# Kernel optimization log

Hardware: AMD Instinct MI355X
Metric: run time of the kernel (lower is better)

The kernel has to match this reference:

```python
import jax, jax.numpy as jnp
import numpy as np
from jax import lax

EPS = 1e-4  # BatchNorm2d eps
K, STRIDE, PAD = 3, 1, 1


def _conv_nchw(x, w, stride, pad):
    return lax.conv_general_dilated(
        x, w, window_strides=(stride, stride), padding=[(pad, pad), (pad, pad)],
        dimension_numbers=("NCHW", "OIHW", "NCHW"))


def setup_inputs() -> dict:
    key = jax.random.key(0)
    ks = jax.random.split(key, 6)
    N, C, H, W = 16, 256, 56, 56
    Cout = 256
    return {
        "x": jax.random.normal(ks[0], (N, C, H, W), jnp.float32),
        "bn_gamma": jax.random.uniform(ks[1], (C,), jnp.float32, 0.5, 1.5),
        "bn_beta": jax.random.normal(ks[2], (C,), jnp.float32) * 0.1,
        "conv_w": jax.random.normal(ks[3], (Cout, C, K, K), jnp.float32) * (1.0 / np.sqrt(C * K * K)),
        "conv_b": jax.random.normal(ks[4], (Cout,), jnp.float32) * 0.01,
        "beta_conv_b": jax.random.normal(ks[5], (1,), jnp.float32) * 0.01,
    }


def reference(x, bn_gamma, bn_beta, conv_w, conv_b, beta_conv_b):
    # --- BatchNorm2d (training-mode batch stats, affine) ---
    mean = jnp.mean(x, axis=(0, 2, 3), keepdims=True)
    var = jnp.mean(jnp.square(x - mean), axis=(0, 2, 3), keepdims=True)  # biased
    xn = (x - mean) * lax.rsqrt(var + EPS)
    xn = xn * bn_gamma[None, :, None, None] + bn_beta[None, :, None, None]

    # --- Ternary quantize (threshold=0; le overwrites ge, so x==0 -> -1) ---
    t = jnp.where(xn >= 0.0, 1.0, 0.0)
    t = jnp.where(xn <= 0.0, -1.0, t).astype(xn.dtype)
    # scale=True, clamp=True
    xc = jnp.clip(xn, -1.0, 1.0)
    c_sum = jnp.sum(xc * t, axis=1, keepdims=True)       # [N,1,H,W]
    c_cnt = jnp.sum(jnp.abs(t), axis=1, keepdims=True)   # L1 norm over channels

    # --- Main conv on ternary activations ---
    y = _conv_nchw(t, conv_w, STRIDE, PAD) + conv_b[None, :, None, None]

    # --- beta: ones-weight box filter (+ beta_conv bias) ---
    ones_k = jnp.ones((1, 1, K, K), x.dtype)
    b_sum = _conv_nchw(c_sum, ones_k, STRIDE, PAD) + beta_conv_b[0]
    b_cnt = _conv_nchw(c_cnt, ones_k, STRIDE, PAD) + beta_conv_b[0]
    beta_map = b_sum / b_cnt                             # [N,1,Ho,Wo]
    return y * beta_map
```

## Files before the change

kernel.cpp:

```cpp
#include <hip/hip_runtime.h>
#include <hip/hip_bf16.h>

typedef __attribute__((ext_vector_type(8))) short bf16x8;
typedef __attribute__((ext_vector_type(4))) float f32x4;

#define NB 16
#define C 256
#define HH 56
#define WW 56
#define HW 3136
#define CHW 802816
#define NPIX 50176
#define PH 58
#define PW 58
#define KTOT 2304
#define PPI 3364
#define NPIXP 53824

#define GLL(g, l) __builtin_amdgcn_global_load_lds( \
    (const __attribute__((address_space(1))) void*)(g), \
    (__attribute__((address_space(3))) void*)(l), 16, 0, 0)

__global__ __launch_bounds__(1024) void stats_kernel(const float* __restrict__ x,
                             const float* __restrict__ gamma, double* __restrict__ stats) {
  int c = blockIdx.x, tid = threadIdx.x;
  double s = 0.0, s2 = 0.0;
  const float* xc = x + (size_t)c * HW;
  for (int k = tid; k < NB * (HW / 4); k += 1024) {
    int n = k / (HW / 4), i = k - n * (HW / 4);
    float4 v = *(const float4*)(xc + (size_t)n * CHW + i * 4);
    double a = v.x, b = v.y, cc = v.z, d = v.w;
    s  += (a + b) + (cc + d);
    s2 += (a * a + b * b) + (cc * cc + d * d);
  }
  __shared__ double rs[1024], rq[1024];
  rs[tid] = s; rq[tid] = s2; __syncthreads();
  for (int o = 512; o > 0; o >>= 1) {
    if (tid < o) { rs[tid] += rs[tid + o]; rq[tid] += rq[tid + o]; }
    __syncthreads();
  }
  if (tid == 0) {
    double mean = rs[0] / (double)NPIX;
    double var = rq[0] / (double)NPIX - mean * mean;
    stats[c] = mean;
    stats[C + c] = (double)gamma[c] / sqrt(var + 1e-4);
  }
}

__global__ __launch_bounds__(256) void ternarize_kernel(const float* __restrict__ x,
                                 const float* __restrict__ beta,
                                 const double* __restrict__ stats,
                                 unsigned short* __restrict__ Tp, float* __restrict__ csum) {
  int bid = blockIdx.x, tid = threadIdx.x;
  int n = bid / HH, h = bid - n * HH;
  __shared__ float xs[256][57];
  const float* xb = x + (size_t)n * CHW + h * WW;
#pragma unroll
  for (int j = 0; j < 14; ++j) {
    int idx = j * 256 + tid;
    int c = idx / 14, q = idx - c * 14;
    float4 v = *(const float4*)(xb + (size_t)c * HW + q * 4);
    float* row = &xs[c][q * 4];
    row[0] = v.x; row[1] = v.y; row[2] = v.z; row[3] = v.w;
  }
  int c8 = tid & 31;
  double mu[8], sc[8], bt[8];
#pragma unroll
  for (int e = 0; e < 8; ++e) {
    int c = c8 + 32 * e;
    mu[e] = stats[c]; sc[e] = stats[C + c]; bt[e] = (double)beta[c];
  }
  __syncthreads();
  unsigned short* tb = Tp + ((size_t)(n * PH + h + 1) * PW + 1) * C;
  float* cs = csum + (size_t)(n * PH + h + 1) * PW + 1;
#pragma unroll
  for (int p = 0; p < 7; ++p) {
    int idx = p * 256 + tid;
    int w = idx >> 5;
    unsigned bits[4];
    float msum = 0.f;
#pragma unroll
    for (int e2 = 0; e2 < 4; ++e2) {
      unsigned lo, hi;
      {
        double xn = ((double)xs[c8 + 64 * e2][w] - mu[2 * e2]) * sc[2 * e2] + bt[2 * e2];
        lo = (xn > 0.0) ? 0x3F80u : 0xBF80u;
        msum += (float)fmin(fabs(xn), 1.0);
      }
      {
        double xn = ((double)xs[c8 + 64 * e2 + 32][w] - mu[2 * e2 + 1]) * sc[2 * e2 + 1] + bt[2 * e2 + 1];
        hi = (xn > 0.0) ? 0x3F80u : 0xBF80u;
        msum += (float)fmin(fabs(xn), 1.0);
      }
      bits[e2] = lo | (hi << 16);
    }
    msum += __shfl_xor(msum, 1); msum += __shfl_xor(msum, 2);
    msum += __shfl_xor(msum, 4); msum += __shfl_xor(msum, 8);
    msum += __shfl_xor(msum, 16);
    uint4 v4; v4.x = bits[0]; v4.y = bits[1]; v4.z = bits[2]; v4.w = bits[3];
    *(uint4*)(tb + (size_t)w * C + c8 * 8) = v4;
    if (c8 == 0) cs[w] = msum;
  }
}

__global__ void prep_kernel(const float* __restrict__ cw, unsigned short* __restrict__ Wp,
                            unsigned short* __restrict__ Tp, float* __restrict__ csum) {
  int b = blockIdx.x, tid = threadIdx.x;
  if (b < 256) {
    int co = b;
    const float* src = cw + (size_t)co * KTOT;
    unsigned short* dst = Wp + (size_t)co * KTOT;
    float v[9];
#pragma unroll
    for (int t9 = 0; t9 < 9; ++t9) v[t9] = src[tid * 9 + t9];
    int p = (tid & 31) * 8 + (tid >> 5);
#pragma unroll
    for (int t9 = 0; t9 < 9; ++t9) {
      unsigned u = __builtin_bit_cast(unsigned, v[t9]);
      unsigned lsb = (u >> 16) & 1u;
      u += 0x7FFFu + lsb;
      dst[t9 * 256 + p] = (unsigned short)(u >> 16);
    }
  } else if (b < 712) {
    int g = (b - 256) * 256 + tid;
    int n = g / 7296; int r = g - n * 7296;
    int pix = r >> 5, c8 = r & 31;
    int h, w;
    if (pix < 58)      { h = 0;  w = pix; }
    else if (pix < 116){ h = 57; w = pix - 58; }
    else { int rem = pix - 116; h = 1 + (rem >> 1); w = (rem & 1) ? 57 : 0; }
    uint4 z = {0u, 0u, 0u, 0u};
    *(uint4*)(Tp + (size_t)((n * PH + h) * PW + w) * C + c8 * 8) = z;
  } else {
    int i = (b - 712) * 256 + tid;
    if (i < NPIXP) csum[i] = 0.f;
  }
}

__global__ __launch_bounds__(512, 2) void conv_kernel(const unsigned short* __restrict__ Wp,
    const unsigned short* __restrict__ Tp, const float* __restrict__ convb,
    const float* __restrict__ csum, const float* __restrict__ betab,
    float* __restrict__ out) {
  int bid = blockIdx.x;
  int ptg = bid >> 5, xcd = bid & 7, ct = (bid >> 3) & 3;
  int pt = ptg * 8 + xcd;
  if (pt >= 106) return;
  int tid = threadIdx.x;
  int co0 = ct * 64;

  __shared__ __align__(16) unsigned short As[2][18432];
  __shared__ __align__(16) unsigned short Bs[2][20480];

  int aofs[5];
#pragma unroll
  for (int r = 0; r < 5; ++r) {
    int lin = r * 512 + tid;
    int co = (lin >> 2) & 63, tap = lin >> 8, pseg = lin & 3;
    int lseg = pseg ^ ((co >> 1) & 3);
    aofs[r] = (co0 + co) * KTOT + tap * 256 + lseg * 8;
  }
  int wstart = pt * 512 - 59;
  int bofs[5];
#pragma unroll
  for (int r = 0; r < 5; ++r) {
    int lin = r * 512 + tid;
    int bpix = lin >> 2, pseg = lin & 3;
    int lseg = pseg ^ ((bpix >> 1) & 3);
    int q = wstart + bpix;
    q = q < 0 ? 0 : (q >= NPIXP ? NPIXP - 1 : q);
    bofs[r] = q * C + lseg * 8;
  }

  int lane = tid & 63, wid = tid >> 6;
  int quad = lane >> 4, row16 = lane & 15;
  int aFoff = row16 * 32 + (quad ^ ((row16 >> 1) & 3)) * 8;
  int pixb = wid * 64 + row16;

  f32x4 acc[4][4];
#pragma unroll
  for (int mi = 0; mi < 4; ++mi)
#pragma unroll
    for (int ni = 0; ni < 4; ++ni)
      acc[mi][ni] = (f32x4){0.f, 0.f, 0.f, 0.f};

#pragma unroll
  for (int r = 0; r < 4; ++r) GLL(Wp + aofs[r], &As[0][(r * 512 + tid) * 8]);
  if (tid < 256)               GLL(Wp + aofs[4], &As[0][(2048 + tid) * 8]);
#pragma unroll
  for (int r = 0; r < 5; ++r) GLL(Tp + bofs[r], &Bs[0][(r * 512 + tid) * 8]);

  for (int s = 0; s < 8; ++s) {
    int cur = s & 1;
    __syncthreads();
    if (s < 7) {
      int c0n = (s + 1) * 32;
#pragma unroll
      for (int r = 0; r < 4; ++r) GLL(Wp + aofs[r] + c0n, &As[cur ^ 1][(r * 512 + tid) * 8]);
      if (tid < 256)               GLL(Wp + aofs[4] + c0n, &As[cur ^ 1][(2048 + tid) * 8]);
#pragma unroll
      for (int r = 0; r < 5; ++r) GLL(Tp + bofs[r] + c0n, &Bs[cur ^ 1][(r * 512 + tid) * 8]);
    }
    const unsigned short* aB = &As[cur][0];
    const unsigned short* bB = &Bs[cur][0];
    __builtin_amdgcn_s_setprio(1);
#pragma unroll
    for (int kh = 0; kh < 3; ++kh) {
#pragma unroll
      for (int kw = 0; kw < 3; ++kw) {
        int tap = kh * 3 + kw;
        bf16x8 a[4], b[4];
#pragma unroll
        for (int mi = 0; mi < 4; ++mi)
          a[mi] = *(const bf16x8*)(aB + tap * 2048 + mi * 512 + aFoff);
#pragma unroll
        for (int ni = 0; ni < 4; ++ni) {
          int pix = pixb + ni * 16 + kh * 58 + kw;
          b[ni] = *(const bf16x8*)(bB + pix * 32 + ((quad ^ ((pix >> 1) & 3)) * 8));
        }
#pragma unroll
        for (int mi = 0; mi < 4; ++mi)
#pragma unroll
          for (int ni = 0; ni < 4; ++ni)
            acc[mi][ni] = __builtin_amdgcn_mfma_f32_16x16x32_bf16(a[mi], b[ni], acc[mi][ni], 0, 0, 0);
      }
    }
    __builtin_amdgcn_s_setprio(0);
  }

  float bb = betab[0];
#pragma unroll
  for (int ni = 0; ni < 4; ++ni) {
    int pp = pt * 512 + wid * 64 + ni * 16 + row16;
    if (pp >= NPIXP) continue;
    int n = pp / PPI; int r2 = pp - n * PPI;
    int ph = r2 / PW;  int pw = r2 - ph * PW;
    if (ph < 1 || ph > 56 || pw < 1 || pw > 56) continue;
    const float* cp = csum + (size_t)(n * PH + ph - 1) * PW + (pw - 1);
    float s9 = 0.f;
#pragma unroll
    for (int i = 0; i < 3; ++i)
#pragma unroll
      for (int j = 0; j < 3; ++j) s9 += cp[i * PW + j];
    int rows = 3 - (ph == 1) - (ph == 56);
    int cols = 3 - (pw == 1) - (pw == 56);
    float bm = (s9 + bb) / (256.0f * (float)(rows * cols) + bb);
    int pix = (ph - 1) * WW + (pw - 1);
    float* ob = out + (size_t)n * CHW + pix;
#pragma unroll
    for (int mi = 0; mi < 4; ++mi) {
      int co = co0 + mi * 16 + quad * 4;
#pragma unroll
      for (int rg = 0; rg < 4; ++rg) {
        ob[(size_t)(co + rg) * HW] = (acc[mi][ni][rg] + convb[co + rg]) * bm;
      }
    }
  }
}

extern "C" void kernel_launch(void* const* d_in, const int* in_sizes, int n_in,
                              void* d_out, int out_size, void* d_ws, size_t ws_size,
                              hipStream_t stream) {
  const float* x     = (const float*)d_in[0];
  const float* gamma = (const float*)d_in[1];
  const float* beta  = (const float*)d_in[2];
  const float* convw = (const float*)d_in[3];
  const float* convb = (const float*)d_in[4];
  const float* betab = (const float*)d_in[5];
  float* out = (float*)d_out;

  char* ws = (char*)d_ws;
  unsigned short* Tp   = (unsigned short*)(ws);
  unsigned short* Wp   = (unsigned short*)(ws + 27557888);
  float*          csum = (float*)(ws + 28737536);
  double*         stats= (double*)(ws + 29153536);

  prep_kernel<<<923, 256, 0, stream>>>(convw, Wp, Tp, csum);
  stats_kernel<<<256, 1024, 0, stream>>>(x, gamma, stats);
  ternarize_kernel<<<896, 256, 0, stream>>>(x, beta, stats, Tp, csum);
  conv_kernel<<<448, 512, 0, stream>>>(Wp, Tp, convb, csum, betab, out);
}
```

Before: 195.7 us.

## Shrink conv tile to 256 pixels with per-kernel-row K staging; merge prep and stats

The conv kernel moves from 512-thread blocks over 512 padded pixels to 256-thread blocks over 256 pixels. The K loop becomes 24 stages, one per kernel row and 32-channel slice, and each stage stages only the three kw taps plus a 320-pixel window. This cuts LDS use per block sharply, raising occupancy and the number of blocks, at the cost of more barriers and more re-fetching of overlapping input rows. Separately, the weight-prep and BN-stats kernels are merged into one launch to remove a kernel launch boundary.

```diff
diff --git a/kernel.cpp b/kernel.cpp
--- a/kernel.cpp
+++ b/kernel.cpp
@@ -21,108 +21,49 @@
     (const __attribute__((address_space(1))) void*)(g), \
     (__attribute__((address_space(3))) void*)(l), 16, 0, 0)
 
-__global__ __launch_bounds__(1024) void stats_kernel(const float* __restrict__ x,
-                             const float* __restrict__ gamma, double* __restrict__ stats) {
-  int c = blockIdx.x, tid = threadIdx.x;
-  double s = 0.0, s2 = 0.0;
-  const float* xc = x + (size_t)c * HW;
-  for (int k = tid; k < NB * (HW / 4); k += 1024) {
-    int n = k / (HW / 4), i = k - n * (HW / 4);
-    float4 v = *(const float4*)(xc + (size_t)n * CHW + i * 4);
-    double a = v.x, b = v.y, cc = v.z, d = v.w;
-    s  += (a + b) + (cc + d);
-    s2 += (a * a + b * b) + (cc * cc + d * d);
-  }
-  __shared__ double rs[1024], rq[1024];
-  rs[tid] = s; rq[tid] = s2; __syncthreads();
-  for (int o = 512; o > 0; o >>= 1) {
-    if (tid < o) { rs[tid] += rs[tid + o]; rq[tid] += rq[tid + o]; }
-    __syncthreads();
-  }
-  if (tid == 0) {
-    double mean = rs[0] / (double)NPIX;
-    double var = rq[0] / (double)NPIX - mean * mean;
-    stats[c] = mean;
-    stats[C + c] = (double)gamma[c] / sqrt(var + 1e-4);
-  }
-}
-
-__global__ __launch_bounds__(256) void ternarize_kernel(const float* __restrict__ x,
-                                 const float* __restrict__ beta,
-                                 const double* __restrict__ stats,
-                                 unsigned short* __restrict__ Tp, float* __restrict__ csum) {
-  int bid = blockIdx.x, tid = threadIdx.x;
-  int n = bid / HH, h = bid - n * HH;
-  __shared__ float xs[256][57];
-  const float* xb = x + (size_t)n * CHW + h * WW;
-#pragma unroll
-  for (int j = 0; j < 14; ++j) {
-    int idx = j * 256 + tid;
-    int c = idx / 14, q = idx - c * 14;
-    float4 v = *(const float4*)(xb + (size_t)c * HW + q * 4);
-    float* row = &xs[c][q * 4];
-    row[0] = v.x; row[1] = v.y; row[2] = v.z; row[3] = v.w;
-  }
-  int c8 = tid & 31;
-  double mu[8], sc[8], bt[8];
-#pragma unroll
-  for (int e = 0; e < 8; ++e) {
-    int c = c8 + 32 * e;
-    mu[e] = stats[c]; sc[e] = stats[C + c]; bt[e] = (double)beta[c];
-  }
-  __syncthreads();
-  unsigned short* tb = Tp + ((size_t)(n * PH + h + 1) * PW + 1) * C;
-  float* cs = csum + (size_t)(n * PH + h + 1) * PW + 1;
-#pragma unroll
-  for (int p = 0; p < 7; ++p) {
-    int idx = p * 256 + tid;
-    int w = idx >> 5;
-    unsigned bits[4];
-    float msum = 0.f;
-#pragma unroll
-    for (int e2 = 0; e2 < 4; ++e2) {
-      unsigned lo, hi;
-      {
-        double xn = ((double)xs[c8 + 64 * e2][w] - mu[2 * e2]) * sc[2 * e2] + bt[2 * e2];
-        lo = (xn > 0.0) ? 0x3F80u : 0xBF80u;
-        msum += (float)fmin(fabs(xn), 1.0);
-      }
-      {
-        double xn = ((double)xs[c8 + 64 * e2 + 32][w] - mu[2 * e2 + 1]) * sc[2 * e2 + 1] + bt[2 * e2 + 1];
-        hi = (xn > 0.0) ? 0x3F80u : 0xBF80u;
-        msum += (float)fmin(fabs(xn), 1.0);
-      }
-      bits[e2] = lo | (hi << 16);
-    }
-    msum += __shfl_xor(msum, 1); msum += __shfl_xor(msum, 2);
-    msum += __shfl_xor(msum, 4); msum += __shfl_xor(msum, 8);
-    msum += __shfl_xor(msum, 16);
-    uint4 v4; v4.x = bits[0]; v4.y = bits[1]; v4.z = bits[2]; v4.w = bits[3];
-    *(uint4*)(tb + (size_t)w * C + c8 * 8) = v4;
-    if (c8 == 0) cs[w] = msum;
-  }
-}
-
-__global__ void prep_kernel(const float* __restrict__ cw, unsigned short* __restrict__ Wp,
-                            unsigned short* __restrict__ Tp, float* __restrict__ csum) {
+__global__ __launch_bounds__(1024) void prep_stats_kernel(const float* __restrict__ x,
+                             const float* __restrict__ gamma, const float* __restrict__ cw,
+                             double* __restrict__ stats, unsigned short* __restrict__ Wp,
+                             unsigned short* __restrict__ Tp, float* __restrict__ csum) {
   int b = blockIdx.x, tid = threadIdx.x;
   if (b < 256) {
-    int co = b;
-    const float* src = cw + (size_t)co * KTOT;
+    int c = b;
+    double s = 0.0, s2 = 0.0;
+    const float* xc = x + (size_t)c * HW;
+    for (int k = tid; k < NB * (HW / 4); k += 1024) {
+      int n = k / (HW / 4), i = k - n * (HW / 4);
+      float4 v = *(const float4*)(xc + (size_t)n * CHW + i * 4);
+      double a = v.x, bb = v.y, cc = v.z, d = v.w;
+      s  += (a + bb) + (cc + d);
+      s2 += (a * a + bb * bb) + (cc * cc + d * d);
+    }
+    __shared__ double rs[1024], rq[1024];
+    rs[tid] = s; rq[tid] = s2; __syncthreads();
+    for (int o = 512; o > 0; o >>= 1) {
+      if (tid < o) { rs[tid] += rs[tid + o]; rq[tid] += rq[tid + o]; }
+      __syncthreads();
+    }
+    if (tid == 0) {
+      double mean = rs[0] / (double)NPIX;
+      double var = rq[0] / (double)NPIX - mean * mean;
+      stats[c] = mean;
+      stats[C + c] = (double)gamma[c] / sqrt(var + 1e-4);
+    }
+  } else if (b < 320) {
+    int co = (b - 256) * 4 + (tid >> 8);
+    int c  = tid & 255;
+    const float* src = cw + (size_t)co * KTOT + c * 9;
     unsigned short* dst = Wp + (size_t)co * KTOT;
-    float v[9];
-#pragma unroll
-    for (int t9 = 0; t9 < 9; ++t9) v[t9] = src[tid * 9 + t9];
-    int p = (tid & 31) * 8 + (tid >> 5);
+    int p = (c & 31) * 8 + (c >> 5);
 #pragma unroll
     for (int t9 = 0; t9 < 9; ++t9) {
-      unsigned u = __builtin_bit_cast(unsigned, v[t9]);
+      unsigned u = __builtin_bit_cast(unsigned, src[t9]);
       unsigned lsb = (u >> 16) & 1u;
       u += 0x7FFFu + lsb;
       dst[t9 * 256 + p] = (unsigned short)(u >> 16);
     }
-  } else if (b < 712) {
-    int g = (b - 256) * 256 + tid;
+  } else if (b < 434) {
+    int g = (b - 320) * 1024 + tid;
     int n = g / 7296; int r = g - n * 7296;
     int pix = r >> 5, c8 = r & 31;
     int h, w;
@@ -132,49 +73,101 @@
     uint4 z = {0u, 0u, 0u, 0u};
     *(uint4*)(Tp + (size_t)((n * PH + h) * PW + w) * C + c8 * 8) = z;
   } else {
-    int i = (b - 712) * 256 + tid;
+    int i = (b - 434) * 1024 + tid;
     if (i < NPIXP) csum[i] = 0.f;
   }
 }
 
-__global__ __launch_bounds__(512, 2) void conv_kernel(const unsigned short* __restrict__ Wp,
+__global__ __launch_bounds__(256) void ternarize_kernel(const float* __restrict__ x,
+                                 const float* __restrict__ beta,
+                                 const double* __restrict__ stats,
+                                 unsigned short* __restrict__ Tp, float* __restrict__ csum) {
+  int bid = blockIdx.x, tid = threadIdx.x;
+  int n = bid / HH, h = bid - n * HH;
+  __shared__ float xs[256][57];
+  const float* xb = x + (size_t)n * CHW + h * WW;
+#pragma unroll
+  for (int j = 0; j < 14; ++j) {
+    int idx = j * 256 + tid;
+    int c = idx / 14, q = idx - c * 14;
+    float4 v = *(const float4*)(xb + (size_t)c * HW + q * 4);
+    float* row = &xs[c][q * 4];
+    row[0] = v.x; row[1] = v.y; row[2] = v.z; row[3] = v.w;
+  }
+  int c8 = tid & 31;
+  double mu[8], sc[8], bt[8];
+#pragma unroll
+  for (int e = 0; e < 8; ++e) {
+    int c = c8 + 32 * e;
+    mu[e] = stats[c]; sc[e] = stats[C + c]; bt[e] = (double)beta[c];
+  }
+  __syncthreads();
+  unsigned short* tb = Tp + ((size_t)(n * PH + h + 1) * PW + 1) * C;
+  float* cs = csum + (size_t)(n * PH + h + 1) * PW + 1;
+#pragma unroll
+  for (int p = 0; p < 7; ++p) {
+    int idx = p * 256 + tid;
+    int w = idx >> 5;
+    unsigned bits[4];
+    float msum = 0.f;
+#pragma unroll
+    for (int e2 = 0; e2 < 4; ++e2) {
+      unsigned lo, hi;
+      {
+        double xn = ((double)xs[c8 + 64 * e2][w] - mu[2 * e2]) * sc[2 * e2] + bt[2 * e2];
+        lo = (xn > 0.0) ? 0x3F80u : 0xBF80u;
+        msum += (float)fmin(fabs(xn), 1.0);
+      }
+      {
+        double xn = ((double)xs[c8 + 64 * e2 + 32][w] - mu[2 * e2 + 1]) * sc[2 * e2 + 1] + bt[2 * e2 + 1];
+        hi = (xn > 0.0) ? 0x3F80u : 0xBF80u;
+        msum += (float)fmin(fabs(xn), 1.0);
+      }
+      bits[e2] = lo | (hi << 16);
+    }
+    msum += __shfl_xor(msum, 1); msum += __shfl_xor(msum, 2);
+    msum += __shfl_xor(msum, 4); msum += __shfl_xor(msum, 8);
+    msum += __shfl_xor(msum, 16);
+    uint4 v4; v4.x = bits[0]; v4.y = bits[1]; v4.z = bits[2]; v4.w = bits[3];
+    *(uint4*)(tb + (size_t)w * C + c8 * 8) = v4;
+    if (c8 == 0) cs[w] = msum;
+  }
+}
+
+__global__ __launch_bounds__(256) void conv_kernel(const unsigned short* __restrict__ Wp,
     const unsigned short* __restrict__ Tp, const float* __restrict__ convb,
     const float* __restrict__ csum, const float* __restrict__ betab,
     float* __restrict__ out) {
   int bid = blockIdx.x;
   int ptg = bid >> 5, xcd = bid & 7, ct = (bid >> 3) & 3;
   int pt = ptg * 8 + xcd;
-  if (pt >= 106) return;
+  if (pt >= 211) return;
   int tid = threadIdx.x;
   int co0 = ct * 64;
 
-  __shared__ __align__(16) unsigned short As[2][18432];
-  __shared__ __align__(16) unsigned short Bs[2][20480];
-
-  int aofs[5];
+  __shared__ __align__(16) unsigned short As[2][3 * 64 * 32];
+  __shared__ __align__(16) unsigned short Bs[2][320 * 32];
+
+  int aofs[3];
+#pragma unroll
+  for (int r = 0; r < 3; ++r) {
+    int lin = r * 256 + tid;
+    int co = (lin >> 2) & 63, tap3 = lin >> 8, pseg = lin & 3;
+    int lseg = pseg ^ ((co >> 1) & 3);
+    aofs[r] = (co0 + co) * KTOT + tap3 * 256 + lseg * 8;
+  }
+  int bpix[5], blseg[5];
 #pragma unroll
   for (int r = 0; r < 5; ++r) {
-    int lin = r * 512 + tid;
-    int co = (lin >> 2) & 63, tap = lin >> 8, pseg = lin & 3;
-    int lseg = pseg ^ ((co >> 1) & 3);
-    aofs[r] = (co0 + co) * KTOT + tap * 256 + lseg * 8;
-  }
-  int wstart = pt * 512 - 59;
-  int bofs[5];
-#pragma unroll
-  for (int r = 0; r < 5; ++r) {
-    int lin = r * 512 + tid;
-    int bpix = lin >> 2, pseg = lin & 3;
-    int lseg = pseg ^ ((bpix >> 1) & 3);
-    int q = wstart + bpix;
-    q = q < 0 ? 0 : (q >= NPIXP ? NPIXP - 1 : q);
-    bofs[r] = q * C + lseg * 8;
+    int lin = r * 256 + tid;
+    bpix[r] = lin >> 2;
+    blseg[r] = (lin & 3) ^ ((bpix[r] >> 1) & 3);
   }
 
   int lane = tid & 63, wid = tid >> 6;
   int quad = lane >> 4, row16 = lane & 15;
   int aFoff = row16 * 32 + (quad ^ ((row16 >> 1) & 3)) * 8;
-  int pixb = wid * 64 + row16;
+  int jbase = wid * 64 + row16 + 31;
 
   f32x4 acc[4][4];
 #pragma unroll
@@ -183,46 +176,54 @@
     for (int ni = 0; ni < 4; ++ni)
       acc[mi][ni] = (f32x4){0.f, 0.f, 0.f, 0.f};
 
-#pragma unroll
-  for (int r = 0; r < 4; ++r) GLL(Wp + aofs[r], &As[0][(r * 512 + tid) * 8]);
-  if (tid < 256)               GLL(Wp + aofs[4], &As[0][(2048 + tid) * 8]);
-#pragma unroll
-  for (int r = 0; r < 5; ++r) GLL(Tp + bofs[r], &Bs[0][(r * 512 + tid) * 8]);
-
-  for (int s = 0; s < 8; ++s) {
+  {
+    int wbase = pt * 256 - 58 - 32;
+#pragma unroll
+    for (int r = 0; r < 3; ++r) GLL(Wp + aofs[r], &As[0][(r * 256 + tid) * 8]);
+#pragma unroll
+    for (int r = 0; r < 5; ++r) {
+      int q = wbase + bpix[r];
+      q = q < 0 ? 0 : (q >= NPIXP ? NPIXP - 1 : q);
+      GLL(Tp + (size_t)q * C + blseg[r] * 8, &Bs[0][(r * 256 + tid) * 8]);
+    }
+  }
+
+  for (int s = 0; s < 24; ++s) {
     int cur = s & 1;
     __syncthreads();
-    if (s < 7) {
-      int c0n = (s + 1) * 32;
-#pragma unroll
-      for (int r = 0; r < 4; ++r) GLL(Wp + aofs[r] + c0n, &As[cur ^ 1][(r * 512 + tid) * 8]);
-      if (tid < 256)               GLL(Wp + aofs[4] + c0n, &As[cur ^ 1][(2048 + tid) * 8]);
-#pragma unroll
-      for (int r = 0; r < 5; ++r) GLL(Tp + bofs[r] + c0n, &Bs[cur ^ 1][(r * 512 + tid) * 8]);
+    if (s < 23) {
+      int s2 = s + 1;
+      int kh2 = s2 >> 3, c2 = (s2 & 7) * 32;
+      int ao = kh2 * 768 + c2;
+#pragma unroll
+      for (int r = 0; r < 3; ++r) GLL(Wp + aofs[r] + ao, &As[cur ^ 1][(r * 256 + tid) * 8]);
+      int wbase2 = pt * 256 + (kh2 - 1) * 58 - 32;
+#pragma unroll
+      for (int r = 0; r < 5; ++r) {
+        int q = wbase2 + bpix[r];
+        q = q < 0 ? 0 : (q >= NPIXP ? NPIXP - 1 : q);
+        GLL(Tp + (size_t)q * C + blseg[r] * 8 + c2, &Bs[cur ^ 1][(r * 256 + tid) * 8]);
+      }
     }
     const unsigned short* aB = &As[cur][0];
     const unsigned short* bB = &Bs[cur][0];
     __builtin_amdgcn_s_setprio(1);
 #pragma unroll
-    for (int kh = 0; kh < 3; ++kh) {
-#pragma unroll
-      for (int kw = 0; kw < 3; ++kw) {
-        int tap = kh * 3 + kw;
-        bf16x8 a[4], b[4];
-#pragma unroll
-        for (int mi = 0; mi < 4; ++mi)
-          a[mi] = *(const bf16x8*)(aB + tap * 2048 + mi * 512 + aFoff);
-#pragma unroll
-        for (int ni = 0; ni < 4; ++ni) {
-          int pix = pixb + ni * 16 + kh * 58 + kw;
-          b[ni] = *(const bf16x8*)(bB + pix * 32 + ((quad ^ ((pix >> 1) & 3)) * 8));
-        }
-#pragma unroll
-        for (int mi = 0; mi < 4; ++mi)
-#pragma unroll
-          for (int ni = 0; ni < 4; ++ni)
-            acc[mi][ni] = __builtin_amdgcn_mfma_f32_16x16x32_bf16(a[mi], b[ni], acc[mi][ni], 0, 0, 0);
-      }
+    for (int kw = 0; kw < 3; ++kw) {
+      bf16x8 a[4], b[4];
+#pragma unroll
+      for (int mi = 0; mi < 4; ++mi)
+        a[mi] = *(const bf16x8*)(aB + kw * 2048 + mi * 512 + aFoff);
+#pragma unroll
+      for (int ni = 0; ni < 4; ++ni) {
+        int pix = jbase + ni * 16 + kw;
+        b[ni] = *(const bf16x8*)(bB + pix * 32 + ((quad ^ ((pix >> 1) & 3)) * 8));
+      }
+#pragma unroll
+      for (int mi = 0; mi < 4; ++mi)
+#pragma unroll
+        for (int ni = 0; ni < 4; ++ni)
+          acc[mi][ni] = __builtin_amdgcn_mfma_f32_16x16x32_bf16(a[mi], b[ni], acc[mi][ni], 0, 0, 0);
     }
     __builtin_amdgcn_s_setprio(0);
   }
@@ -230,7 +231,7 @@
   float bb = betab[0];
 #pragma unroll
   for (int ni = 0; ni < 4; ++ni) {
-    int pp = pt * 512 + wid * 64 + ni * 16 + row16;
+    int pp = pt * 256 + wid * 64 + ni * 16 + row16;
     if (pp >= NPIXP) continue;
     int n = pp / PPI; int r2 = pp - n * PPI;
     int ph = r2 / PW;  int pw = r2 - ph * PW;
@@ -274,8 +275,7 @@
   float*          csum = (float*)(ws + 28737536);
   double*         stats= (double*)(ws + 29153536);
 
-  prep_kernel<<<923, 256, 0, stream>>>(convw, Wp, Tp, csum);
-  stats_kernel<<<256, 1024, 0, stream>>>(x, gamma, stats);
+  prep_stats_kernel<<<487, 1024, 0, stream>>>(x, gamma, convw, stats, Wp, Tp, csum);
   ternarize_kernel<<<896, 256, 0, stream>>>(x, beta, stats, Tp, csum);
-  conv_kernel<<<448, 512, 0, stream>>>(Wp, Tp, convb, csum, betab, out);
-}
+  conv_kernel<<<864, 256, 0, stream>>>(Wp, Tp, convb, csum, betab, out);
+}
```

Result: slower. 201.9 us (+3.1%).
